# Kernel tuning notes

Hardware: AMD Instinct MI355X
Metric: run time of the kernel (lower is better)

Reference implementation:

```python
import jax, jax.numpy as jnp
import numpy as np

N_NODES = 65536
IN_FEAT = 512
OUT_FEAT = 256
N_REL = 3
N_EDGES = 500000
NEG_SLOPE = 0.2  # DGL GATConv default
EPS = 1e-9


def setup_inputs() -> dict:
    key = jax.random.key(0)
    ks = jax.random.split(key, 7)
    h = jax.random.normal(ks[0], (N_NODES, IN_FEAT), dtype=jnp.float32)
    # Glorot-ish scaling keeps attention logits in a sane range
    W = jax.random.normal(ks[1], (N_REL, IN_FEAT, OUT_FEAT), dtype=jnp.float32) / np.sqrt(IN_FEAT)
    attn_l = jax.random.normal(ks[2], (N_REL, OUT_FEAT), dtype=jnp.float32) / np.sqrt(OUT_FEAT)
    attn_r = jax.random.normal(ks[3], (N_REL, OUT_FEAT), dtype=jnp.float32) / np.sqrt(OUT_FEAT)
    b = jnp.zeros((N_REL, OUT_FEAT), dtype=jnp.float32)
    src = jax.random.randint(ks[4], (N_REL, N_EDGES), 0, N_NODES, dtype=jnp.int32)
    dst = jax.random.randint(ks[5], (N_REL, N_EDGES), 0, N_NODES, dtype=jnp.int32)
    return {"h": h, "W": W, "attn_l": attn_l, "attn_r": attn_r, "b": b, "src": src, "dst": dst}


def _gat_relation(h, W_r, al_r, ar_r, b_r, src_r, dst_r):
    n = h.shape[0]
    z = h @ W_r                                  # [N, F_out] dense projection
    el = z @ al_r                                # [N] per-node left logit
    er = z @ ar_r                                # [N] per-node right logit
    e = jax.nn.leaky_relu(el[src_r] + er[dst_r], NEG_SLOPE)  # [E]
    # edge_softmax over incoming edges of each destination node
    m = jax.ops.segment_max(e, dst_r, num_segments=n)        # [N]
    w = jnp.exp(e - m[dst_r])                                # [E]
    denom = jax.ops.segment_sum(w, dst_r, num_segments=n)    # [N]
    alpha = w / (denom[dst_r] + EPS)                         # [E]
    out = jax.ops.segment_sum(alpha[:, None] * z[src_r], dst_r, num_segments=n)
    return out + b_r


def reference(h, W, attn_l, attn_r, b, src, dst):
    n_rel = W.shape[0]
    out = jnp.zeros((h.shape[0], W.shape[2]), dtype=h.dtype)
    # HeteroGraphConv default aggregate='sum' over relations; num_heads=1 then squeeze
    for r in range(n_rel):
        out = out + _gat_relation(h, W[r], attn_l[r], attn_r[r], b[r], src[r], dst[r])
    return out
```

## Files before the change

kernel.cpp:

```cpp
#include <hip/hip_runtime.h>
#include <hip/hip_bf16.h>
#include <cstdint>
#include <cstddef>

#define N_NODES 65536
#define IN_FEAT 512
#define OUT_FEAT 256
#define N_REL 3
#define TOT_EDGES (N_REL * 500000)
#define N_EDGES 500000
#define NEG_SLOPE 0.2f
#define EPS_F 1e-9f
#define BK 64

typedef __bf16 bf16x8 __attribute__((ext_vector_type(8)));
typedef float f32x4 __attribute__((ext_vector_type(4)));

__device__ __forceinline__ void async16(const void* g, void* l) {
    __builtin_amdgcn_global_load_lds(
        (const __attribute__((address_space(1))) unsigned int*)g,
        (__attribute__((address_space(3))) unsigned int*)l, 16, 0, 0);
}

__global__ __launch_bounds__(256) void kPrep(
    const float* __restrict__ W,
    __bf16* __restrict__ Wt,
    float* __restrict__ el, float* __restrict__ er, int* __restrict__ head) {
    __shared__ float tile[64][65];
    const int b = blockIdx.x;
    const int t = threadIdx.x;
    if (b < 768) {
        int i = b * 256 + t;
        el[i] = 0.f;
        er[i] = 0.f;
        head[i] = -1;
    } else {
        int b2 = b - 768;
        int r = b2 >> 5;
        int kt = (b2 >> 2) & 7;
        int nt = b2 & 3;
        int k0 = kt * 64, n0 = nt * 64;
        int trow = t >> 6, tcol = t & 63;
        const float* Wr = W + (size_t)r * IN_FEAT * OUT_FEAT;
#pragma unroll
        for (int p = 0; p < 16; p++) {
            int k = p * 4 + trow;
            tile[k][tcol] = Wr[(size_t)(k0 + k) * OUT_FEAT + n0 + tcol];
        }
        __syncthreads();
        __bf16* Wtr = Wt + (size_t)r * OUT_FEAT * IN_FEAT;
#pragma unroll
        for (int p = 0; p < 16; p++) {
            int n = p * 4 + trow;
            Wtr[(size_t)(n0 + n) * IN_FEAT + k0 + tcol] = (__bf16)tile[tcol][n];
        }
    }
}

__global__ __launch_bounds__(256, 2) void kGemm(
    const float* __restrict__ h, const __bf16* __restrict__ Wt,
    const float* __restrict__ attn_l, const float* __restrict__ attn_r,
    __bf16* __restrict__ z, float* __restrict__ el, float* __restrict__ er) {
    __shared__ __bf16 Al[128 * BK];
    __shared__ __bf16 Bl[256 * BK];
    const int bid = blockIdx.x;
    const int xcd = bid & 7;
    const int slot = bid >> 3;
    const int mt6 = slot / 3;
    const int r = slot - mt6 * 3;
    const int m_base = (xcd * 64 + mt6) * 128;

    const int t = threadIdx.x;
    const int lane = t & 63;
    const int wave = t >> 6;
    const int wm = wave >> 1, wn = wave & 1;
    const int colL = lane & 15, quad = lane >> 4;

    const __bf16* WtR = Wt + (size_t)r * OUT_FEAT * IN_FEAT;

    f32x4 acc[4][8];
#pragma unroll
    for (int mt = 0; mt < 4; mt++)
#pragma unroll
        for (int nt = 0; nt < 8; nt++) acc[mt][nt] = (f32x4){0.f, 0.f, 0.f, 0.f};

    for (int k0 = 0; k0 < IN_FEAT; k0 += BK) {
        if (k0) __syncthreads();
#pragma unroll
        for (int i = 0; i < 8; i++) {
            int s = i * 256 + t;
            int n = s >> 3, cp = s & 7, cs = cp ^ (n & 7);
            const __bf16* g = WtR + (size_t)n * IN_FEAT + k0 + cs * 8;
            __bf16* l = Bl + (size_t)(i * 256 + (wave << 6)) * 8;
            async16(g, l);
        }
#pragma unroll
        for (int i = 0; i < 4; i++) {
            int s = i * 256 + t;
            int row = s >> 3, cp = s & 7, cs = cp ^ (row & 7);
            const float* g = h + (size_t)(m_base + row) * IN_FEAT + k0 + cs * 8;
            float4 v0 = ((const float4*)g)[0];
            float4 v1 = ((const float4*)g)[1];
            bf16x8 w;
            w[0] = (__bf16)v0.x; w[1] = (__bf16)v0.y; w[2] = (__bf16)v0.z; w[3] = (__bf16)v0.w;
            w[4] = (__bf16)v1.x; w[5] = (__bf16)v1.y; w[6] = (__bf16)v1.z; w[7] = (__bf16)v1.w;
            *(bf16x8*)(Al + (size_t)s * 8) = w;
        }
        __syncthreads();
#pragma unroll
        for (int kk = 0; kk < 2; kk++) {
            const int cbase = kk * 4 + quad;
            bf16x8 af[4], bfr[8];
#pragma unroll
            for (int mt = 0; mt < 4; mt++) {
                int row = wm * 64 + mt * 16 + colL;
                int cp = cbase ^ (row & 7);
                af[mt] = *(const bf16x8*)(Al + (size_t)((row << 3) + cp) * 8);
            }
#pragma unroll
            for (int nt = 0; nt < 8; nt++) {
                int n = wn * 128 + nt * 16 + colL;
                int cp = cbase ^ (n & 7);
                bfr[nt] = *(const bf16x8*)(Bl + (size_t)((n << 3) + cp) * 8);
            }
#pragma unroll
            for (int mt = 0; mt < 4; mt++)
#pragma unroll
                for (int nt = 0; nt < 8; nt++)
                    acc[mt][nt] = __builtin_amdgcn_mfma_f32_16x16x32_bf16(
                        af[mt], bfr[nt], acc[mt][nt], 0, 0, 0);
        }
    }

    const float* alv = attn_l + r * OUT_FEAT;
    const float* arv = attn_r + r * OUT_FEAT;
    __bf16* zr = z + (size_t)r * N_NODES * OUT_FEAT;
    float elp[4][4], erp[4][4];
#pragma unroll
    for (int mt = 0; mt < 4; mt++)
#pragma unroll
        for (int q = 0; q < 4; q++) { elp[mt][q] = 0.f; erp[mt][q] = 0.f; }
#pragma unroll
    for (int mt = 0; mt < 4; mt++) {
#pragma unroll
        for (int nt = 0; nt < 8; nt++) {
            int c = wn * 128 + nt * 16 + colL;
            float al = alv[c], ar = arv[c];
#pragma unroll
            for (int q = 0; q < 4; q++) {
                float v = acc[mt][nt][q];
                int row = m_base + wm * 64 + mt * 16 + quad * 4 + q;
                zr[(size_t)row * OUT_FEAT + c] = (__bf16)v;
                elp[mt][q] += v * al;
                erp[mt][q] += v * ar;
            }
        }
    }
#pragma unroll
    for (int mt = 0; mt < 4; mt++)
#pragma unroll
        for (int q = 0; q < 4; q++) {
#pragma unroll
            for (int off = 1; off < 16; off <<= 1) {
                elp[mt][q] += __shfl_xor(elp[mt][q], off, 64);
                erp[mt][q] += __shfl_xor(erp[mt][q], off, 64);
            }
        }
    if (colL == 0) {
#pragma unroll
        for (int mt = 0; mt < 4; mt++)
#pragma unroll
            for (int q = 0; q < 4; q++) {
                int row = m_base + wm * 64 + mt * 16 + quad * 4 + q;
                atomicAdd(el + r * N_NODES + row, elp[mt][q]);
                atomicAdd(er + r * N_NODES + row, erp[mt][q]);
            }
    }
}

__global__ void kLink(const int* __restrict__ dst, const int* __restrict__ srcArr,
                      int* __restrict__ head, int2* __restrict__ next2) {
    int i = blockIdx.x * blockDim.x + threadIdx.x;
    if (i >= TOT_EDGES) return;
    int r = i / N_EDGES;
    int d = dst[i];
    int prev = atomicExch(head + r * N_NODES + d, i);
    next2[i] = make_int2(prev, srcArr[i]);
}

__global__ __launch_bounds__(192) void kAgg(
    const __bf16* __restrict__ z, const int* __restrict__ head,
    const int2* __restrict__ next2,
    const float* __restrict__ el, const float* __restrict__ er,
    const float* __restrict__ bias, float* __restrict__ out) {
    __shared__ float cm[12][256];
    const int t = threadIdx.x;
    const int wv = t >> 6;
    const int lane = t & 63;
    const int half = lane >> 5;
    const int l = lane & 31;
    const int hw = wv * 2 + half;
    const int nl = (hw >= 3) ? 1 : 0;
    const int r = hw - nl * 3;
    const int nodeA = blockIdx.x * 4 + nl;
    const int nodeB = nodeA + 2;
    const int idxA = r * N_NODES + nodeA;
    const int idxB = r * N_NODES + nodeB;

    const float ervA = er[idxA];
    const float ervB = er[idxB];
    const float* elr = el + r * N_NODES;
    const uint4* zrel = (const uint4*)(z + (size_t)r * N_NODES * OUT_FEAT);

    float a0 = 0.f, a1 = 0.f, a2 = 0.f, a3 = 0.f;
    float a4 = 0.f, a5 = 0.f, a6 = 0.f, a7 = 0.f;
    float b0 = 0.f, b1 = 0.f, b2 = 0.f, b3 = 0.f;
    float b4 = 0.f, b5 = 0.f, b6 = 0.f, b7 = 0.f;
    float wsumA = 0.f, wsumB = 0.f;
    int curA = head[idxA];
    int curB = head[idxB];
    while (curA >= 0 || curB >= 0) {
        int2 nsA, nsB;
        const bool doA = curA >= 0, doB = curB >= 0;
        if (doA) nsA = next2[curA];
        if (doB) nsB = next2[curB];
        if (doA) {
            int s = nsA.y;
            float x = elr[s] + ervA;
            x = x > 0.f ? x : NEG_SLOPE * x;
            float w = __expf(x);
            uint4 v = zrel[(size_t)s * 32 + l];
            wsumA += w;
            a0 += w * __uint_as_float(v.x << 16);
            a1 += w * __uint_as_float(v.x & 0xFFFF0000u);
            a2 += w * __uint_as_float(v.y << 16);
            a3 += w * __uint_as_float(v.y & 0xFFFF0000u);
            a4 += w * __uint_as_float(v.z << 16);
            a5 += w * __uint_as_float(v.z & 0xFFFF0000u);
            a6 += w * __uint_as_float(v.w << 16);
            a7 += w * __uint_as_float(v.w & 0xFFFF0000u);
            curA = nsA.x;
        }
        if (doB) {
            int s = nsB.y;
            float x = elr[s] + ervB;
            x = x > 0.f ? x : NEG_SLOPE * x;
            float w = __expf(x);
            uint4 v = zrel[(size_t)s * 32 + l];
            wsumB += w;
            b0 += w * __uint_as_float(v.x << 16);
            b1 += w * __uint_as_float(v.x & 0xFFFF0000u);
            b2 += w * __uint_as_float(v.y << 16);
            b3 += w * __uint_as_float(v.y & 0xFFFF0000u);
            b4 += w * __uint_as_float(v.z << 16);
            b5 += w * __uint_as_float(v.z & 0xFFFF0000u);
            b6 += w * __uint_as_float(v.w << 16);
            b7 += w * __uint_as_float(v.w & 0xFFFF0000u);
            curB = nsB.x;
        }
    }
    {
        float invd = 1.f / (wsumA + EPS_F);
        float* cr = &cm[hw][l * 8];
        *(float4*)cr       = make_float4(a0 * invd, a1 * invd, a2 * invd, a3 * invd);
        *(float4*)(cr + 4) = make_float4(a4 * invd, a5 * invd, a6 * invd, a7 * invd);
    }
    {
        float invd = 1.f / (wsumB + EPS_F);
        float* cr = &cm[6 + hw][l * 8];
        *(float4*)cr       = make_float4(b0 * invd, b1 * invd, b2 * invd, b3 * invd);
        *(float4*)(cr + 4) = make_float4(b4 * invd, b5 * invd, b6 * invd, b7 * invd);
    }
    __syncthreads();

    if (hw < 4) {
        const int c = l * 8;
        const float* r0 = &cm[hw * 3 + 0][c];
        const float* r1 = &cm[hw * 3 + 1][c];
        const float* r2 = &cm[hw * 3 + 2][c];
        const float* q0 = bias + c;
        const float* q1 = bias + OUT_FEAT + c;
        const float* q2 = bias + 2 * OUT_FEAT + c;
        float f0 = r0[0] + r1[0] + r2[0] + q0[0] + q1[0] + q2[0];
        float f1 = r0[1] + r1[1] + r2[1] + q0[1] + q1[1] + q2[1];
        float f2 = r0[2] + r1[2] + r2[2] + q0[2] + q1[2] + q2[2];
        float f3 = r0[3] + r1[3] + r2[3] + q0[3] + q1[3] + q2[3];
        float f4 = r0[4] + r1[4] + r2[4] + q0[4] + q1[4] + q2[4];
        float f5 = r0[5] + r1[5] + r2[5] + q0[5] + q1[5] + q2[5];
        float f6 = r0[6] + r1[6] + r2[6] + q0[6] + q1[6] + q2[6];
        float f7 = r0[7] + r1[7] + r2[7] + q0[7] + q1[7] + q2[7];
        const int node = blockIdx.x * 4 + hw;
        float* orow = out + (size_t)node * OUT_FEAT + c;
        *(float4*)orow       = make_float4(f0, f1, f2, f3);
        *(float4*)(orow + 4) = make_float4(f4, f5, f6, f7);
    }
}

extern "C" void kernel_launch(void* const* d_in, const int* in_sizes, int n_in,
                              void* d_out, int out_size, void* d_ws, size_t ws_size,
                              hipStream_t stream) {
    const float* h      = (const float*)d_in[0];
    const float* W      = (const float*)d_in[1];
    const float* attn_l = (const float*)d_in[2];
    const float* attn_r = (const float*)d_in[3];
    const float* bias   = (const float*)d_in[4];
    const int*   src    = (const int*)d_in[5];
    const int*   dst    = (const int*)d_in[6];
    float* out = (float*)d_out;
    char* ws = (char*)d_ws;

    size_t off_b = 0;
    auto alloc = [&](size_t bytes) {
        size_t o = off_b;
        off_b = (off_b + bytes + 255) & ~(size_t)255;
        return o;
    };
    size_t oZ    = alloc((size_t)N_REL * N_NODES * OUT_FEAT * 2);
    size_t oWT   = alloc((size_t)N_REL * OUT_FEAT * IN_FEAT * 2);
    size_t oEL   = alloc((size_t)N_REL * N_NODES * 4);
    size_t oER   = alloc((size_t)N_REL * N_NODES * 4);
    size_t oHEAD = alloc((size_t)N_REL * N_NODES * 4);
    size_t oNEXT = alloc((size_t)TOT_EDGES * 8);

    __bf16* z     = (__bf16*)(ws + oZ);
    __bf16* Wt    = (__bf16*)(ws + oWT);
    float*  el    = (float*)(ws + oEL);
    float*  er    = (float*)(ws + oER);
    int*    head  = (int*)(ws + oHEAD);
    int2*   next2 = (int2*)(ws + oNEXT);

    kPrep<<<864, 256, 0, stream>>>(W, Wt, el, er, head);
    kLink<<<(TOT_EDGES + 255) / 256, 256, 0, stream>>>(dst, src, head, next2);
    kGemm<<<1536, 256, 0, stream>>>(h, Wt, attn_l, attn_r, z, el, er);
    kAgg<<<N_NODES / 4, 192, 0, stream>>>(z, head, next2, el, er, bias, out);
}
```

Measured before the change: 495.4 us.

## Double-buffer GEMM with larger 256-row tiles and simplify aggregation to one chain

The projection GEMM now uses 512-thread blocks with 256x256 output tiles and BK=32, double-buffering the LDS tiles so the next k-slice loads while MFMAs run on the current one. The aggregation kernel drops the interleaved two-node chain walk, so each half-wave follows one linked list and twice as many blocks are launched. The GEMM change targets load latency and the per-k-step synchronisation, at the cost of more registers per thread, which may limit occupancy. The aggregation change removes the memory-level parallelism the paired chains gave and may lengthen the dependent pointer-chasing latency.

```diff
diff --git a/kernel.cpp b/kernel.cpp
--- a/kernel.cpp
+++ b/kernel.cpp
@@ -11,7 +11,7 @@
 #define N_EDGES 500000
 #define NEG_SLOPE 0.2f
 #define EPS_F 1e-9f
-#define BK 64
+#define BK 32
 
 typedef __bf16 bf16x8 __attribute__((ext_vector_type(8)));
 typedef float f32x4 __attribute__((ext_vector_type(4)));
@@ -57,99 +57,138 @@
     }
 }
 
-__global__ __launch_bounds__(256, 2) void kGemm(
+__global__ __launch_bounds__(512, 2) void kGemm(
     const float* __restrict__ h, const __bf16* __restrict__ Wt,
     const float* __restrict__ attn_l, const float* __restrict__ attn_r,
     __bf16* __restrict__ z, float* __restrict__ el, float* __restrict__ er) {
-    __shared__ __bf16 Al[128 * BK];
-    __shared__ __bf16 Bl[256 * BK];
+    __shared__ __bf16 Al[2][256 * BK];
+    __shared__ __bf16 Bl[2][256 * BK];
+
     const int bid = blockIdx.x;
     const int xcd = bid & 7;
     const int slot = bid >> 3;
-    const int mt6 = slot / 3;
-    const int r = slot - mt6 * 3;
-    const int m_base = (xcd * 64 + mt6) * 128;
+    const int mtg = slot / 3;
+    const int r = slot - mtg * 3;
+    const int m_base = (xcd * 32 + mtg) * 256;
 
     const int t = threadIdx.x;
     const int lane = t & 63;
     const int wave = t >> 6;
-    const int wm = wave >> 1, wn = wave & 1;
+    const int wm = wave >> 2;
+    const int wn = wave & 3;
     const int colL = lane & 15, quad = lane >> 4;
 
     const __bf16* WtR = Wt + (size_t)r * OUT_FEAT * IN_FEAT;
 
-    f32x4 acc[4][8];
-#pragma unroll
-    for (int mt = 0; mt < 4; mt++)
-#pragma unroll
-        for (int nt = 0; nt < 8; nt++) acc[mt][nt] = (f32x4){0.f, 0.f, 0.f, 0.f};
-
-    for (int k0 = 0; k0 < IN_FEAT; k0 += BK) {
-        if (k0) __syncthreads();
-#pragma unroll
-        for (int i = 0; i < 8; i++) {
-            int s = i * 256 + t;
-            int n = s >> 3, cp = s & 7, cs = cp ^ (n & 7);
-            const __bf16* g = WtR + (size_t)n * IN_FEAT + k0 + cs * 8;
-            __bf16* l = Bl + (size_t)(i * 256 + (wave << 6)) * 8;
-            async16(g, l);
-        }
-#pragma unroll
-        for (int i = 0; i < 4; i++) {
-            int s = i * 256 + t;
-            int row = s >> 3, cp = s & 7, cs = cp ^ (row & 7);
-            const float* g = h + (size_t)(m_base + row) * IN_FEAT + k0 + cs * 8;
+    f32x4 acc[8][4];
+#pragma unroll
+    for (int mt = 0; mt < 8; mt++)
+#pragma unroll
+        for (int nt = 0; nt < 4; nt++) acc[mt][nt] = (f32x4){0.f, 0.f, 0.f, 0.f};
+
+
+    {
+#pragma unroll
+        for (int i = 0; i < 2; i++) {
+            int s = i * 512 + t;
+            int n = s >> 2, cp = s & 3, cs = cp ^ (n & 3);
+            const __bf16* g = WtR + (size_t)n * IN_FEAT + cs * 8;
+            async16(g, (__bf16*)Bl[0] + (size_t)s * 8);
+        }
+#pragma unroll
+        for (int i = 0; i < 2; i++) {
+            int s = i * 512 + t;
+            int row = s >> 2, cp = s & 3, cs = cp ^ (row & 3);
+            const float* g = h + (size_t)(m_base + row) * IN_FEAT + cs * 8;
             float4 v0 = ((const float4*)g)[0];
             float4 v1 = ((const float4*)g)[1];
             bf16x8 w;
             w[0] = (__bf16)v0.x; w[1] = (__bf16)v0.y; w[2] = (__bf16)v0.z; w[3] = (__bf16)v0.w;
             w[4] = (__bf16)v1.x; w[5] = (__bf16)v1.y; w[6] = (__bf16)v1.z; w[7] = (__bf16)v1.w;
-            *(bf16x8*)(Al + (size_t)s * 8) = w;
-        }
-        __syncthreads();
-#pragma unroll
-        for (int kk = 0; kk < 2; kk++) {
-            const int cbase = kk * 4 + quad;
-            bf16x8 af[4], bfr[8];
-#pragma unroll
-            for (int mt = 0; mt < 4; mt++) {
-                int row = wm * 64 + mt * 16 + colL;
-                int cp = cbase ^ (row & 7);
-                af[mt] = *(const bf16x8*)(Al + (size_t)((row << 3) + cp) * 8);
-            }
-#pragma unroll
-            for (int nt = 0; nt < 8; nt++) {
-                int n = wn * 128 + nt * 16 + colL;
-                int cp = cbase ^ (n & 7);
-                bfr[nt] = *(const bf16x8*)(Bl + (size_t)((n << 3) + cp) * 8);
-            }
-#pragma unroll
-            for (int mt = 0; mt < 4; mt++)
-#pragma unroll
-                for (int nt = 0; nt < 8; nt++)
+            *(bf16x8*)((__bf16*)Al[0] + (size_t)s * 8) = w;
+        }
+    }
+    __syncthreads();
+
+    const int NSTEP = IN_FEAT / BK;
+    for (int step = 0; step < NSTEP; ++step) {
+        const int cur = step & 1, nxt = cur ^ 1;
+        const int k1 = (step + 1) * BK;
+        float4 a0[2], a1[2];
+        const bool more = (step + 1) < NSTEP;
+        if (more) {
+#pragma unroll
+            for (int i = 0; i < 2; i++) {
+                int s = i * 512 + t;
+                int n = s >> 2, cp = s & 3, cs = cp ^ (n & 3);
+                const __bf16* g = WtR + (size_t)n * IN_FEAT + k1 + cs * 8;
+                async16(g, (__bf16*)Bl[nxt] + (size_t)s * 8);
+            }
+#pragma unroll
+            for (int i = 0; i < 2; i++) {
+                int s = i * 512 + t;
+                int row = s >> 2, cp = s & 3, cs = cp ^ (row & 3);
+                const float* g = h + (size_t)(m_base + row) * IN_FEAT + k1 + cs * 8;
+                a0[i] = ((const float4*)g)[0];
+                a1[i] = ((const float4*)g)[1];
+            }
+        }
+        {
+            const __bf16* Ab = (const __bf16*)Al[cur];
+            const __bf16* Bb = (const __bf16*)Bl[cur];
+            bf16x8 af[8], bfr[4];
+#pragma unroll
+            for (int mt = 0; mt < 8; mt++) {
+                int row = wm * 128 + mt * 16 + colL;
+                int cp = quad ^ (row & 3);
+                af[mt] = *(const bf16x8*)(Ab + (size_t)((row << 2) + cp) * 8);
+            }
+#pragma unroll
+            for (int nt = 0; nt < 4; nt++) {
+                int n = wn * 64 + nt * 16 + colL;
+                int cp = quad ^ (n & 3);
+                bfr[nt] = *(const bf16x8*)(Bb + (size_t)((n << 2) + cp) * 8);
+            }
+#pragma unroll
+            for (int mt = 0; mt < 8; mt++)
+#pragma unroll
+                for (int nt = 0; nt < 4; nt++)
                     acc[mt][nt] = __builtin_amdgcn_mfma_f32_16x16x32_bf16(
                         af[mt], bfr[nt], acc[mt][nt], 0, 0, 0);
         }
+        if (more) {
+#pragma unroll
+            for (int i = 0; i < 2; i++) {
+                int s = i * 512 + t;
+                bf16x8 w;
+                w[0] = (__bf16)a0[i].x; w[1] = (__bf16)a0[i].y;
+                w[2] = (__bf16)a0[i].z; w[3] = (__bf16)a0[i].w;
+                w[4] = (__bf16)a1[i].x; w[5] = (__bf16)a1[i].y;
+                w[6] = (__bf16)a1[i].z; w[7] = (__bf16)a1[i].w;
+                *(bf16x8*)((__bf16*)Al[nxt] + (size_t)s * 8) = w;
+            }
+        }
+        __syncthreads();
     }
 
     const float* alv = attn_l + r * OUT_FEAT;
     const float* arv = attn_r + r * OUT_FEAT;
     __bf16* zr = z + (size_t)r * N_NODES * OUT_FEAT;
-    float elp[4][4], erp[4][4];
-#pragma unroll
-    for (int mt = 0; mt < 4; mt++)
+    float elp[8][4], erp[8][4];
+#pragma unroll
+    for (int mt = 0; mt < 8; mt++)
 #pragma unroll
         for (int q = 0; q < 4; q++) { elp[mt][q] = 0.f; erp[mt][q] = 0.f; }
 #pragma unroll
-    for (int mt = 0; mt < 4; mt++) {
-#pragma unroll
-        for (int nt = 0; nt < 8; nt++) {
-            int c = wn * 128 + nt * 16 + colL;
+    for (int mt = 0; mt < 8; mt++) {
+#pragma unroll
+        for (int nt = 0; nt < 4; nt++) {
+            int c = wn * 64 + nt * 16 + colL;
             float al = alv[c], ar = arv[c];
 #pragma unroll
             for (int q = 0; q < 4; q++) {
                 float v = acc[mt][nt][q];
-                int row = m_base + wm * 64 + mt * 16 + quad * 4 + q;
+                int row = m_base + wm * 128 + mt * 16 + quad * 4 + q;
                 zr[(size_t)row * OUT_FEAT + c] = (__bf16)v;
                 elp[mt][q] += v * al;
                 erp[mt][q] += v * ar;
@@ -157,7 +196,7 @@
         }
     }
 #pragma unroll
-    for (int mt = 0; mt < 4; mt++)
+    for (int mt = 0; mt < 8; mt++)
 #pragma unroll
         for (int q = 0; q < 4; q++) {
 #pragma unroll
@@ -168,10 +207,10 @@
         }
     if (colL == 0) {
 #pragma unroll
-        for (int mt = 0; mt < 4; mt++)
+        for (int mt = 0; mt < 8; mt++)
 #pragma unroll
             for (int q = 0; q < 4; q++) {
-                int row = m_base + wm * 64 + mt * 16 + quad * 4 + q;
+                int row = m_base + wm * 128 + mt * 16 + quad * 4 + q;
                 atomicAdd(el + r * N_NODES + row, elp[mt][q]);
                 atomicAdd(er + r * N_NODES + row, erp[mt][q]);
             }
@@ -193,7 +232,7 @@
     const int2* __restrict__ next2,
     const float* __restrict__ el, const float* __restrict__ er,
     const float* __restrict__ bias, float* __restrict__ out) {
-    __shared__ float cm[12][256];
+    __shared__ float cm[6][256];
     const int t = threadIdx.x;
     const int wv = t >> 6;
     const int lane = t & 63;
@@ -202,94 +241,57 @@
     const int hw = wv * 2 + half;
     const int nl = (hw >= 3) ? 1 : 0;
     const int r = hw - nl * 3;
-    const int nodeA = blockIdx.x * 4 + nl;
-    const int nodeB = nodeA + 2;
-    const int idxA = r * N_NODES + nodeA;
-    const int idxB = r * N_NODES + nodeB;
-
-    const float ervA = er[idxA];
-    const float ervB = er[idxB];
+    const int node = blockIdx.x * 2 + nl;
+    const int idx = r * N_NODES + node;
+
+    const float erv = er[idx];
     const float* elr = el + r * N_NODES;
     const uint4* zrel = (const uint4*)(z + (size_t)r * N_NODES * OUT_FEAT);
 
-    float a0 = 0.f, a1 = 0.f, a2 = 0.f, a3 = 0.f;
-    float a4 = 0.f, a5 = 0.f, a6 = 0.f, a7 = 0.f;
-    float b0 = 0.f, b1 = 0.f, b2 = 0.f, b3 = 0.f;
-    float b4 = 0.f, b5 = 0.f, b6 = 0.f, b7 = 0.f;
-    float wsumA = 0.f, wsumB = 0.f;
-    int curA = head[idxA];
-    int curB = head[idxB];
-    while (curA >= 0 || curB >= 0) {
-        int2 nsA, nsB;
-        const bool doA = curA >= 0, doB = curB >= 0;
-        if (doA) nsA = next2[curA];
-        if (doB) nsB = next2[curB];
-        if (doA) {
-            int s = nsA.y;
-            float x = elr[s] + ervA;
-            x = x > 0.f ? x : NEG_SLOPE * x;
-            float w = __expf(x);
-            uint4 v = zrel[(size_t)s * 32 + l];
-            wsumA += w;
-            a0 += w * __uint_as_float(v.x << 16);
-            a1 += w * __uint_as_float(v.x & 0xFFFF0000u);
-            a2 += w * __uint_as_float(v.y << 16);
-            a3 += w * __uint_as_float(v.y & 0xFFFF0000u);
-            a4 += w * __uint_as_float(v.z << 16);
-            a5 += w * __uint_as_float(v.z & 0xFFFF0000u);
-            a6 += w * __uint_as_float(v.w << 16);
-            a7 += w * __uint_as_float(v.w & 0xFFFF0000u);
-            curA = nsA.x;
-        }
-        if (doB) {
-            int s = nsB.y;
-            float x = elr[s] + ervB;
-            x = x > 0.f ? x : NEG_SLOPE * x;
-            float w = __expf(x);
-            uint4 v = zrel[(size_t)s * 32 + l];
-            wsumB += w;
-            b0 += w * __uint_as_float(v.x << 16);
-            b1 += w * __uint_as_float(v.x & 0xFFFF0000u);
-            b2 += w * __uint_as_float(v.y << 16);
-            b3 += w * __uint_as_float(v.y & 0xFFFF0000u);
-            b4 += w * __uint_as_float(v.z << 16);
-            b5 += w * __uint_as_float(v.z & 0xFFFF0000u);
-            b6 += w * __uint_as_float(v.w << 16);
-            b7 += w * __uint_as_float(v.w & 0xFFFF0000u);
-            curB = nsB.x;
-        }
-    }
-    {
-        float invd = 1.f / (wsumA + EPS_F);
-        float* cr = &cm[hw][l * 8];
-        *(float4*)cr       = make_float4(a0 * invd, a1 * invd, a2 * invd, a3 * invd);
-        *(float4*)(cr + 4) = make_float4(a4 * invd, a5 * invd, a6 * invd, a7 * invd);
-    }
-    {
-        float invd = 1.f / (wsumB + EPS_F);
-        float* cr = &cm[6 + hw][l * 8];
-        *(float4*)cr       = make_float4(b0 * invd, b1 * invd, b2 * invd, b3 * invd);
-        *(float4*)(cr + 4) = make_float4(b4 * invd, b5 * invd, b6 * invd, b7 * invd);
-    }
+    float p0 = 0.f, p1 = 0.f, p2 = 0.f, p3 = 0.f;
+    float p4 = 0.f, p5 = 0.f, p6 = 0.f, p7 = 0.f;
+    float wsum = 0.f;
+    int cur = head[idx];
+    while (cur >= 0) {
+        int2 ns = next2[cur];
+        int s = ns.y;
+        float x = elr[s] + erv;
+        x = x > 0.f ? x : NEG_SLOPE * x;
+        float w = __expf(x);
+        uint4 v = zrel[(size_t)s * 32 + l];
+        wsum += w;
+        p0 += w * __uint_as_float(v.x << 16);
+        p1 += w * __uint_as_float(v.x & 0xFFFF0000u);
+        p2 += w * __uint_as_float(v.y << 16);
+        p3 += w * __uint_as_float(v.y & 0xFFFF0000u);
+        p4 += w * __uint_as_float(v.z << 16);
+        p5 += w * __uint_as_float(v.z & 0xFFFF0000u);
+        p6 += w * __uint_as_float(v.w << 16);
+        p7 += w * __uint_as_float(v.w & 0xFFFF0000u);
+        cur = ns.x;
+    }
+    float invd = 1.f / (wsum + EPS_F);
+    float* cr = &cm[hw][l * 8];
+    *(float4*)cr       = make_float4(p0 * invd, p1 * invd, p2 * invd, p3 * invd);
+    *(float4*)(cr + 4) = make_float4(p4 * invd, p5 * invd, p6 * invd, p7 * invd);
     __syncthreads();
 
-    if (hw < 4) {
+    if (r == 0) {
         const int c = l * 8;
-        const float* r0 = &cm[hw * 3 + 0][c];
-        const float* r1 = &cm[hw * 3 + 1][c];
-        const float* r2 = &cm[hw * 3 + 2][c];
-        const float* q0 = bias + c;
-        const float* q1 = bias + OUT_FEAT + c;
-        const float* q2 = bias + 2 * OUT_FEAT + c;
-        float f0 = r0[0] + r1[0] + r2[0] + q0[0] + q1[0] + q2[0];
-        float f1 = r0[1] + r1[1] + r2[1] + q0[1] + q1[1] + q2[1];
-        float f2 = r0[2] + r1[2] + r2[2] + q0[2] + q1[2] + q2[2];
-        float f3 = r0[3] + r1[3] + r2[3] + q0[3] + q1[3] + q2[3];
-        float f4 = r0[4] + r1[4] + r2[4] + q0[4] + q1[4] + q2[4];
-        float f5 = r0[5] + r1[5] + r2[5] + q0[5] + q1[5] + q2[5];
-        float f6 = r0[6] + r1[6] + r2[6] + q0[6] + q1[6] + q2[6];
-        float f7 = r0[7] + r1[7] + r2[7] + q0[7] + q1[7] + q2[7];
-        const int node = blockIdx.x * 4 + hw;
+        const float* r0 = &cm[nl * 3 + 0][c];
+        const float* r1 = &cm[nl * 3 + 1][c];
+        const float* r2 = &cm[nl * 3 + 2][c];
+        const float* b0 = bias + c;
+        const float* b1 = bias + OUT_FEAT + c;
+        const float* b2 = bias + 2 * OUT_FEAT + c;
+        float f0 = r0[0] + r1[0] + r2[0] + b0[0] + b1[0] + b2[0];
+        float f1 = r0[1] + r1[1] + r2[1] + b0[1] + b1[1] + b2[1];
+        float f2 = r0[2] + r1[2] + r2[2] + b0[2] + b1[2] + b2[2];
+        float f3 = r0[3] + r1[3] + r2[3] + b0[3] + b1[3] + b2[3];
+        float f4 = r0[4] + r1[4] + r2[4] + b0[4] + b1[4] + b2[4];
+        float f5 = r0[5] + r1[5] + r2[5] + b0[5] + b1[5] + b2[5];
+        float f6 = r0[6] + r1[6] + r2[6] + b0[6] + b1[6] + b2[6];
+        float f7 = r0[7] + r1[7] + r2[7] + b0[7] + b1[7] + b2[7];
         float* orow = out + (size_t)node * OUT_FEAT + c;
         *(float4*)orow       = make_float4(f0, f1, f2, f3);
         *(float4*)(orow + 4) = make_float4(f4, f5, f6, f7);
@@ -331,6 +333,6 @@
 
     kPrep<<<864, 256, 0, stream>>>(W, Wt, el, er, head);
     kLink<<<(TOT_EDGES + 255) / 256, 256, 0, stream>>>(dst, src, head, next2);
-    kGemm<<<1536, 256, 0, stream>>>(h, Wt, attn_l, attn_r, z, el, er);
-    kAgg<<<N_NODES / 4, 192, 0, stream>>>(z, head, next2, el, er, bias, out);
-}
+    kGemm<<<768, 512, 0, stream>>>(h, Wt, attn_l, attn_r, z, el, er);
+    kAgg<<<N_NODES / 2, 192, 0, stream>>>(z, head, next2, el, er, bias, out);
+}
```

New measurement: 522.5 us. 1.05x slower.

## Fuse edge-linking into GEMM launch and simplify aggregation to one node per half-wave

Applied to the files above, without the earlier changes.

Appends the linked-list construction blocks to the GEMM grid so both run in one launch and the atomic edge linking can overlap with the matrix projection. The aggregation kernel drops the two-node interleaved list walk and gives each half-wave a single node, doubling the grid and halving shared memory. This loses the memory-level parallelism that came from walking two independent chains at once, but removes a launch and the divergence between the two chains.

```diff
diff --git a/kernel.cpp b/kernel.cpp
--- a/kernel.cpp
+++ b/kernel.cpp
@@ -12,6 +12,9 @@
 #define NEG_SLOPE 0.2f
 #define EPS_F 1e-9f
 #define BK 64
+
+#define NB_GEMM 1536
+#define NB_LINK ((TOT_EDGES + 255) / 256)
 
 typedef __bf16 bf16x8 __attribute__((ext_vector_type(8)));
 typedef float f32x4 __attribute__((ext_vector_type(4)));
@@ -57,20 +60,34 @@
     }
 }
 
-__global__ __launch_bounds__(256, 2) void kGemm(
+__global__ __launch_bounds__(256, 2) void kGemmLink(
     const float* __restrict__ h, const __bf16* __restrict__ Wt,
     const float* __restrict__ attn_l, const float* __restrict__ attn_r,
-    __bf16* __restrict__ z, float* __restrict__ el, float* __restrict__ er) {
+    __bf16* __restrict__ z, float* __restrict__ el, float* __restrict__ er,
+    const int* __restrict__ dst, const int* __restrict__ srcArr,
+    int* __restrict__ head, int2* __restrict__ next2) {
     __shared__ __bf16 Al[128 * BK];
     __shared__ __bf16 Bl[256 * BK];
     const int bid = blockIdx.x;
+    const int t = threadIdx.x;
+
+    if (bid >= NB_GEMM) {
+        int i = (bid - NB_GEMM) * 256 + t;
+        if (i < TOT_EDGES) {
+            int r = i / N_EDGES;
+            int d = dst[i];
+            int prev = atomicExch(head + r * N_NODES + d, i);
+            next2[i] = make_int2(prev, srcArr[i]);
+        }
+        return;
+    }
+
     const int xcd = bid & 7;
     const int slot = bid >> 3;
     const int mt6 = slot / 3;
     const int r = slot - mt6 * 3;
     const int m_base = (xcd * 64 + mt6) * 128;
 
-    const int t = threadIdx.x;
     const int lane = t & 63;
     const int wave = t >> 6;
     const int wm = wave >> 1, wn = wave & 1;
@@ -178,22 +195,12 @@
     }
 }
 
-__global__ void kLink(const int* __restrict__ dst, const int* __restrict__ srcArr,
-                      int* __restrict__ head, int2* __restrict__ next2) {
-    int i = blockIdx.x * blockDim.x + threadIdx.x;
-    if (i >= TOT_EDGES) return;
-    int r = i / N_EDGES;
-    int d = dst[i];
-    int prev = atomicExch(head + r * N_NODES + d, i);
-    next2[i] = make_int2(prev, srcArr[i]);
-}
-
 __global__ __launch_bounds__(192) void kAgg(
     const __bf16* __restrict__ z, const int* __restrict__ head,
     const int2* __restrict__ next2,
     const float* __restrict__ el, const float* __restrict__ er,
     const float* __restrict__ bias, float* __restrict__ out) {
-    __shared__ float cm[12][256];
+    __shared__ float cm[6][256];
     const int t = threadIdx.x;
     const int wv = t >> 6;
     const int lane = t & 63;
@@ -202,94 +209,57 @@
     const int hw = wv * 2 + half;
     const int nl = (hw >= 3) ? 1 : 0;
     const int r = hw - nl * 3;
-    const int nodeA = blockIdx.x * 4 + nl;
-    const int nodeB = nodeA + 2;
-    const int idxA = r * N_NODES + nodeA;
-    const int idxB = r * N_NODES + nodeB;
-
-    const float ervA = er[idxA];
-    const float ervB = er[idxB];
+    const int node = blockIdx.x * 2 + nl;
+    const int idx = r * N_NODES + node;
+
+    const float erv = er[idx];
     const float* elr = el + r * N_NODES;
     const uint4* zrel = (const uint4*)(z + (size_t)r * N_NODES * OUT_FEAT);
 
-    float a0 = 0.f, a1 = 0.f, a2 = 0.f, a3 = 0.f;
-    float a4 = 0.f, a5 = 0.f, a6 = 0.f, a7 = 0.f;
-    float b0 = 0.f, b1 = 0.f, b2 = 0.f, b3 = 0.f;
-    float b4 = 0.f, b5 = 0.f, b6 = 0.f, b7 = 0.f;
-    float wsumA = 0.f, wsumB = 0.f;
-    int curA = head[idxA];
-    int curB = head[idxB];
-    while (curA >= 0 || curB >= 0) {
-        int2 nsA, nsB;
-        const bool doA = curA >= 0, doB = curB >= 0;
-        if (doA) nsA = next2[curA];
-        if (doB) nsB = next2[curB];
-        if (doA) {
-            int s = nsA.y;
-            float x = elr[s] + ervA;
-            x = x > 0.f ? x : NEG_SLOPE * x;
-            float w = __expf(x);
-            uint4 v = zrel[(size_t)s * 32 + l];
-            wsumA += w;
-            a0 += w * __uint_as_float(v.x << 16);
-            a1 += w * __uint_as_float(v.x & 0xFFFF0000u);
-            a2 += w * __uint_as_float(v.y << 16);
-            a3 += w * __uint_as_float(v.y & 0xFFFF0000u);
-            a4 += w * __uint_as_float(v.z << 16);
-            a5 += w * __uint_as_float(v.z & 0xFFFF0000u);
-            a6 += w * __uint_as_float(v.w << 16);
-            a7 += w * __uint_as_float(v.w & 0xFFFF0000u);
-            curA = nsA.x;
-        }
-        if (doB) {
-            int s = nsB.y;
-            float x = elr[s] + ervB;
-            x = x > 0.f ? x : NEG_SLOPE * x;
-            float w = __expf(x);
-            uint4 v = zrel[(size_t)s * 32 + l];
-            wsumB += w;
-            b0 += w * __uint_as_float(v.x << 16);
-            b1 += w * __uint_as_float(v.x & 0xFFFF0000u);
-            b2 += w * __uint_as_float(v.y << 16);
-            b3 += w * __uint_as_float(v.y & 0xFFFF0000u);
-            b4 += w * __uint_as_float(v.z << 16);
-            b5 += w * __uint_as_float(v.z & 0xFFFF0000u);
-            b6 += w * __uint_as_float(v.w << 16);
-            b7 += w * __uint_as_float(v.w & 0xFFFF0000u);
-            curB = nsB.x;
-        }
-    }
-    {
-        float invd = 1.f / (wsumA + EPS_F);
-        float* cr = &cm[hw][l * 8];
-        *(float4*)cr       = make_float4(a0 * invd, a1 * invd, a2 * invd, a3 * invd);
-        *(float4*)(cr + 4) = make_float4(a4 * invd, a5 * invd, a6 * invd, a7 * invd);
-    }
-    {
-        float invd = 1.f / (wsumB + EPS_F);
-        float* cr = &cm[6 + hw][l * 8];
-        *(float4*)cr       = make_float4(b0 * invd, b1 * invd, b2 * invd, b3 * invd);
-        *(float4*)(cr + 4) = make_float4(b4 * invd, b5 * invd, b6 * invd, b7 * invd);
-    }
+    float p0 = 0.f, p1 = 0.f, p2 = 0.f, p3 = 0.f;
+    float p4 = 0.f, p5 = 0.f, p6 = 0.f, p7 = 0.f;
+    float wsum = 0.f;
+    int cur = head[idx];
+    while (cur >= 0) {
+        int2 ns = next2[cur];
+        int s = ns.y;
+        float x = elr[s] + erv;
+        x = x > 0.f ? x : NEG_SLOPE * x;
+        float w = __expf(x);
+        uint4 v = zrel[(size_t)s * 32 + l];
+        wsum += w;
+        p0 += w * __uint_as_float(v.x << 16);
+        p1 += w * __uint_as_float(v.x & 0xFFFF0000u);
+        p2 += w * __uint_as_float(v.y << 16);
+        p3 += w * __uint_as_float(v.y & 0xFFFF0000u);
+        p4 += w * __uint_as_float(v.z << 16);
+        p5 += w * __uint_as_float(v.z & 0xFFFF0000u);
+        p6 += w * __uint_as_float(v.w << 16);
+        p7 += w * __uint_as_float(v.w & 0xFFFF0000u);
+        cur = ns.x;
+    }
+    float invd = 1.f / (wsum + EPS_F);
+    float* cr = &cm[hw][l * 8];
+    *(float4*)cr       = make_float4(p0 * invd, p1 * invd, p2 * invd, p3 * invd);
+    *(float4*)(cr + 4) = make_float4(p4 * invd, p5 * invd, p6 * invd, p7 * invd);
     __syncthreads();
 
-    if (hw < 4) {
+    if (r == 0) {
         const int c = l * 8;
-        const float* r0 = &cm[hw * 3 + 0][c];
-        const float* r1 = &cm[hw * 3 + 1][c];
-        const float* r2 = &cm[hw * 3 + 2][c];
-        const float* q0 = bias + c;
-        const float* q1 = bias + OUT_FEAT + c;
-        const float* q2 = bias + 2 * OUT_FEAT + c;
-        float f0 = r0[0] + r1[0] + r2[0] + q0[0] + q1[0] + q2[0];
-        float f1 = r0[1] + r1[1] + r2[1] + q0[1] + q1[1] + q2[1];
-        float f2 = r0[2] + r1[2] + r2[2] + q0[2] + q1[2] + q2[2];
-        float f3 = r0[3] + r1[3] + r2[3] + q0[3] + q1[3] + q2[3];
-        float f4 = r0[4] + r1[4] + r2[4] + q0[4] + q1[4] + q2[4];
-        float f5 = r0[5] + r1[5] + r2[5] + q0[5] + q1[5] + q2[5];
-        float f6 = r0[6] + r1[6] + r2[6] + q0[6] + q1[6] + q2[6];
-        float f7 = r0[7] + r1[7] + r2[7] + q0[7] + q1[7] + q2[7];
-        const int node = blockIdx.x * 4 + hw;
+        const float* r0 = &cm[nl * 3 + 0][c];
+        const float* r1 = &cm[nl * 3 + 1][c];
+        const float* r2 = &cm[nl * 3 + 2][c];
+        const float* b0 = bias + c;
+        const float* b1 = bias + OUT_FEAT + c;
+        const float* b2 = bias + 2 * OUT_FEAT + c;
+        float f0 = r0[0] + r1[0] + r2[0] + b0[0] + b1[0] + b2[0];
+        float f1 = r0[1] + r1[1] + r2[1] + b0[1] + b1[1] + b2[1];
+        float f2 = r0[2] + r1[2] + r2[2] + b0[2] + b1[2] + b2[2];
+        float f3 = r0[3] + r1[3] + r2[3] + b0[3] + b1[3] + b2[3];
+        float f4 = r0[4] + r1[4] + r2[4] + b0[4] + b1[4] + b2[4];
+        float f5 = r0[5] + r1[5] + r2[5] + b0[5] + b1[5] + b2[5];
+        float f6 = r0[6] + r1[6] + r2[6] + b0[6] + b1[6] + b2[6];
+        float f7 = r0[7] + r1[7] + r2[7] + b0[7] + b1[7] + b2[7];
         float* orow = out + (size_t)node * OUT_FEAT + c;
         *(float4*)orow       = make_float4(f0, f1, f2, f3);
         *(float4*)(orow + 4) = make_float4(f4, f5, f6, f7);
@@ -330,7 +300,7 @@
     int2*   next2 = (int2*)(ws + oNEXT);
 
     kPrep<<<864, 256, 0, stream>>>(W, Wt, el, er, head);
-    kLink<<<(TOT_EDGES + 255) / 256, 256, 0, stream>>>(dst, src, head, next2);
-    kGemm<<<1536, 256, 0, stream>>>(h, Wt, attn_l, attn_r, z, el, er);
-    kAgg<<<N_NODES / 4, 192, 0, stream>>>(z, head, next2, el, er, bias, out);
-}
+    kGemmLink<<<NB_GEMM + NB_LINK, 256, 0, stream>>>(
+        h, Wt, attn_l, attn_r, z, el, er, dst, src, head, next2);
+    kAgg<<<N_NODES / 2, 192, 0, stream>>>(z, head, next2, el, er, bias, out);
+}
```

Measured after the change: 476.3 us. 3.9% less time.
